# Performance work log

Hardware: AMD Instinct MI355X
Metric: run time of the kernel (lower is better)

## Reference

```python
import jax, jax.numpy as jnp
import numpy as np

B, T, D, H = 64, 256, 512, 512
COMB = D + H + D  # x, h, mask concatenated


def setup_inputs() -> dict:
    key = jax.random.key(0)
    ks = jax.random.split(key, 16)
    s = 1.0 / np.sqrt(COMB)
    sd = 1.0 / np.sqrt(D)
    inp = {
        "x": jax.random.normal(ks[0], (B, 4, T, D), dtype=jnp.float32),
        "X_mean": jax.random.normal(ks[1], (T, D), dtype=jnp.float32),
        # gate linears: stored as [in, out] so we do comb @ W + b
        "Wi": jax.random.uniform(ks[2], (COMB, H), minval=-s, maxval=s),
        "bi": jax.random.uniform(ks[3], (H,), minval=-s, maxval=s),
        "Wf": jax.random.uniform(ks[4], (COMB, H), minval=-s, maxval=s),
        "bf": jax.random.uniform(ks[5], (H,), minval=-s, maxval=s),
        "Wo": jax.random.uniform(ks[6], (COMB, H), minval=-s, maxval=s),
        "bo": jax.random.uniform(ks[7], (H,), minval=-s, maxval=s),
        "Wc": jax.random.uniform(ks[8], (COMB, H), minval=-s, maxval=s),
        "bc": jax.random.uniform(ks[9], (H,), minval=-s, maxval=s),
        # gamma_x_l: FilterLinear with identity filter -> diagonal weight + bias
        "gx_w": jax.random.uniform(ks[10], (D,), minval=-sd, maxval=sd),
        "gx_b": jax.random.uniform(ks[11], (D,), minval=-sd, maxval=sd),
        # gamma_h_l: full linear D -> D, stored [in, out]
        "gh_W": jax.random.uniform(ks[12], (D, D), minval=-sd, maxval=sd),
        "gh_b": jax.random.uniform(ks[13], (D,), minval=-sd, maxval=sd),
    }
    return inp


def _forward(x, X_mean, Wi, bi, Wf, bf, Wo, bo, Wc, bc, gx_w, gx_b, gh_W, gh_b):
    # split the packed input: each [T, B, D] for scan
    X = jnp.transpose(x[:, 0], (1, 0, 2))
    Xl = jnp.transpose(x[:, 1], (1, 0, 2))
    M = jnp.transpose(x[:, 2], (1, 0, 2))
    Dl = jnp.transpose(x[:, 3], (1, 0, 2))

    h0 = jnp.zeros((x.shape[0], H), dtype=x.dtype)
    c0 = jnp.zeros((x.shape[0], H), dtype=x.dtype)

    def step(carry, inp):
        h, c = carry
        xt, xl, m, dl, xm = inp  # xm: [D]
        delta_x = jnp.exp(-jnp.maximum(0.0, dl * gx_w + gx_b))
        delta_h = jnp.exp(-jnp.maximum(0.0, dl @ gh_W + gh_b))
        xt = m * xt + (1.0 - m) * (delta_x * xl + (1.0 - delta_x) * xm)
        h = delta_h * h
        comb = jnp.concatenate([xt, h, m], axis=-1)  # [B, COMB]
        i = jax.nn.sigmoid(comb @ Wi + bi)
        f = jax.nn.sigmoid(comb @ Wf + bf)
        o = jax.nn.sigmoid(comb @ Wo + bo)
        c_tilde = jnp.tanh(comb @ Wc + bc)
        c = f * c + i * c_tilde
        h = o * jnp.tanh(c)
        return (h, c), h

    _, outs = jax.lax.scan(step, (h0, c0), (X, Xl, M, Dl, X_mean))
    return jnp.transpose(outs, (1, 0, 2))  # [B, T, H]


def reference(x, X_mean, Wi, bi, Wf, bf, Wo, bo, Wc, bc, gx_w, gx_b, gh_W, gh_b):
    return _forward(x, X_mean, Wi, bi, Wf, bf, Wo, bo, Wc, bc, gx_w, gx_b, gh_W, gh_b)
```

## Files before the change

kernel.cpp:

```cpp
#include <hip/hip_runtime.h>
#include <hip/hip_fp16.h>
#include <math.h>

#define TT 256
#define BB 64
#define DD 512
#define HH 512
#define NC 2048

#define AH_OFF   0ull
#define DLH_OFF  8388608ull
#define DH_OFF   12582912ull
#define GP_OFF   20971520ull
#define WCT_OFF  37748736ull
#define GHT_OFF  38797312ull
#define WHT_OFF  38928384ull
#define BC_OFF   39452672ull
#define HS_OFF   39454720ull
#define FLG_OFF  39487488ull

typedef _Float16 h8_t __attribute__((ext_vector_type(8)));
typedef _Float16 h4_t __attribute__((ext_vector_type(4)));
typedef float f32x4 __attribute__((ext_vector_type(4)));
typedef unsigned long long ull2_t __attribute__((ext_vector_type(2)));

typedef const __attribute__((address_space(1))) void* gas_p;
typedef __attribute__((address_space(3))) void* las_p;

__device__ __forceinline__ float fast_exp2(float x) {
#if defined(__has_builtin)
#if __has_builtin(__builtin_amdgcn_exp2f)
  return __builtin_amdgcn_exp2f(x);
#else
  return exp2f(x);
#endif
#else
  return exp2f(x);
#endif
}
__device__ __forceinline__ float fast_rcp(float x) {
#if defined(__has_builtin)
#if __has_builtin(__builtin_amdgcn_rcpf)
  return __builtin_amdgcn_rcpf(x);
#else
  return 1.0f / x;
#endif
#else
  return 1.0f / x;
#endif
}
#define LOG2E 1.4426950408889634f
__device__ __forceinline__ float sigmoidf_(float v) {
  return fast_rcp(1.0f + fast_exp2(-LOG2E * v));
}
__device__ __forceinline__ float tanhf_(float v) {
  return 1.0f - 2.0f * fast_rcp(1.0f + fast_exp2(2.0f * LOG2E * v));
}

__global__ __launch_bounds__(256) void prep_kernel(
    const float* __restrict__ x, const float* __restrict__ Xmean,
    const float* __restrict__ gxw, const float* __restrict__ gxb,
    __half* __restrict__ AH, __half* __restrict__ DLh,
    const float* __restrict__ Wi, const float* __restrict__ bi,
    const float* __restrict__ Wf, const float* __restrict__ bff,
    const float* __restrict__ Wo, const float* __restrict__ bo,
    const float* __restrict__ Wc, const float* __restrict__ bc,
    const float* __restrict__ ghW,
    __half* __restrict__ WCT, __half* __restrict__ WHT,
    __half* __restrict__ GHT, float* __restrict__ BC,
    unsigned* __restrict__ HS) {
  const int bx = blockIdx.x;
  const int tid = threadIdx.x;

  if (bx < 8192) {
    int idx = bx * 256 + tid;
    int d = (idx & 127) * 4;
    int r = idx >> 7;
    int b = r & 63, t = r >> 6;
    size_t base = (((size_t)b * 4) * TT + t) * DD + d;
    const float4 X = *(const float4*)&x[base];
    const float4 Xl = *(const float4*)&x[base + (size_t)TT * DD];
    const float4 M = *(const float4*)&x[base + 2ull * TT * DD];
    const float4 Dl = *(const float4*)&x[base + 3ull * TT * DD];
    const float4 xm = *(const float4*)&Xmean[(size_t)t * DD + d];
    const float4 gw = *(const float4*)&gxw[d];
    const float4 gb = *(const float4*)&gxb[d];
    float o[4];
    {
      float dx = fast_exp2(-LOG2E * fmaxf(0.f, Dl.x * gw.x + gb.x));
      o[0] = M.x * X.x + (1.f - M.x) * (dx * Xl.x + (1.f - dx) * xm.x);
    }
    {
      float dx = fast_exp2(-LOG2E * fmaxf(0.f, Dl.y * gw.y + gb.y));
      o[1] = M.y * X.y + (1.f - M.y) * (dx * Xl.y + (1.f - dx) * xm.y);
    }
    {
      float dx = fast_exp2(-LOG2E * fmaxf(0.f, Dl.z * gw.z + gb.z));
      o[2] = M.z * X.z + (1.f - M.z) * (dx * Xl.z + (1.f - dx) * xm.z);
    }
    {
      float dx = fast_exp2(-LOG2E * fmaxf(0.f, Dl.w * gw.w + gb.w));
      o[3] = M.w * X.w + (1.f - M.w) * (dx * Xl.w + (1.f - dx) * xm.w);
    }
    h4_t xo = {(_Float16)o[0], (_Float16)o[1], (_Float16)o[2], (_Float16)o[3]};
    h4_t mo = {(_Float16)M.x, (_Float16)M.y, (_Float16)M.z, (_Float16)M.w};
    h4_t dlo = {(_Float16)Dl.x, (_Float16)Dl.y, (_Float16)Dl.z, (_Float16)Dl.w};
    *(h4_t*)&AH[(size_t)r * 1024 + d] = xo;
    *(h4_t*)&AH[(size_t)r * 1024 + 512 + d] = mo;
    *(h4_t*)&DLh[(size_t)r * 512 + d] = dlo;
    return;
  }

  if (bx == 9025) {
    for (int i = tid; i < 32832; i += 256) HS[i] = 0u;
    return;
  }

  const int rbx = bx - 8192;
  if (rbx == 832) {
    const float* bs[4] = {bi, bff, bo, bc};
    for (int j = tid; j < 512; j += 256)
#pragma unroll
      for (int g = 0; g < 4; ++g) BC[j * 4 + g] = bs[g][j];
    return;
  }
  __shared__ _Float16 tl[64][68];
  const int p = rbx % 13;
  const int tile = rbx / 13;
  const int k0 = (tile >> 3) << 6, j0 = (tile & 7) << 6;
  const float* Ws[4] = {Wi, Wf, Wo, Wc};

  const float* src;
  size_t koff;
  __half* dst;
  int dstride, dkoff, g = 0;
  if (p < 12) {
    g = p & 3;
    const int part = p >> 2;
    src = Ws[g];
    koff = (part == 0) ? 0 : (part == 1 ? 1024 : 512);
    if (part == 2) { dst = WHT; dstride = 512; dkoff = 0; }
    else           { dst = WCT; dstride = 1024; dkoff = (part == 1) ? 512 : 0; }
  } else {
    src = ghW; koff = 0; dst = GHT; dstride = 512; dkoff = 0;
  }

  const int jj = tid & 63, kr = tid >> 6;
#pragma unroll
  for (int r = 0; r < 16; ++r) {
    const int kk = r * 4 + kr;
    tl[jj][kk] = (_Float16)src[(koff + k0 + kk) * 512 + (j0 + jj)];
  }
  __syncthreads();

  const int c4 = (tid & 15) * 4;
#pragma unroll
  for (int pass = 0; pass < 4; ++pass) {
    const int jj2 = (tid >> 4) + pass * 16;
    const h4_t v = *(const h4_t*)&tl[jj2][c4];
    size_t idx;
    if (p < 12)
      idx = (size_t)(4 * (j0 + jj2) + g) * dstride + dkoff + k0 + c4;
    else
      idx = (size_t)(j0 + jj2) * 512 + k0 + c4;
    *(h4_t*)&dst[idx] = v;
  }
}

__device__ __forceinline__ void gemm_body(
    _Float16* Ash, _Float16* Bsh,
    const __half* __restrict__ A, const __half* __restrict__ BT,
    const float* __restrict__ bias, void* __restrict__ C,
    int K, int Ncols, int mode, int id, int nblk) {
  const int tid = threadIdx.x;
  const int lane = tid & 63, w = tid >> 6;
  const int l15 = lane & 15, quad = lane >> 4;
  const int wr = w >> 1, wc = w & 1;

  const int nx = Ncols >> 7;
  const int ny = nblk / nx;
  const int ysl = ny >> 3;
  const int xcd = id & 7;
  const int q = id >> 3;
  const int row0 = (xcd * ysl + (q % ysl)) * 128;
  const int col0 = (q / ysl) * 128;

  f32x4 acc[4][4] = {};

  const int ci0 = tid, ci1 = 256 + tid;
  const int ar0 = ci0 >> 2, ac0 = (ci0 & 3) * 8;
  const int ar1 = ci1 >> 2, ac1 = (ci1 & 3) * 8;
  const __half* Abase = A + (size_t)row0 * K;
  const __half* Bbase = BT + (size_t)col0 * K;

  for (int k0 = 0; k0 < K; k0 += 32) {
    __syncthreads();
    __builtin_amdgcn_global_load_lds((gas_p)(Abase + (size_t)ar0 * K + k0 + ac0),
                                     (las_p)(Ash + ci0 * 8), 16, 0, 0);
    __builtin_amdgcn_global_load_lds((gas_p)(Abase + (size_t)ar1 * K + k0 + ac1),
                                     (las_p)(Ash + ci1 * 8), 16, 0, 0);
    __builtin_amdgcn_global_load_lds((gas_p)(Bbase + (size_t)ar0 * K + k0 + ac0),
                                     (las_p)(Bsh + ci0 * 8), 16, 0, 0);
    __builtin_amdgcn_global_load_lds((gas_p)(Bbase + (size_t)ar1 * K + k0 + ac1),
                                     (las_p)(Bsh + ci1 * 8), 16, 0, 0);
    __syncthreads();
    h8_t af[4], bf[4];
#pragma unroll
    for (int mt = 0; mt < 4; ++mt)
      af[mt] = *(const h8_t*)&Ash[(wr * 64 + mt * 16 + l15) * 32 + quad * 8];
#pragma unroll
    for (int ct = 0; ct < 4; ++ct)
      bf[ct] = *(const h8_t*)&Bsh[(wc * 64 + ct * 16 + l15) * 32 + quad * 8];
#pragma unroll
    for (int mt = 0; mt < 4; ++mt)
#pragma unroll
      for (int ct = 0; ct < 4; ++ct)
        acc[mt][ct] = __builtin_amdgcn_mfma_f32_16x16x32_f16(af[mt], bf[ct], acc[mt][ct], 0, 0, 0);
  }

#pragma unroll
  for (int ct = 0; ct < 4; ++ct) {
    const int col = col0 + wc * 64 + ct * 16 + l15;
    const float bv = bias[col];
#pragma unroll
    for (int mt = 0; mt < 4; ++mt) {
#pragma unroll
      for (int reg = 0; reg < 4; ++reg) {
        const int row = row0 + wr * 64 + mt * 16 + quad * 4 + reg;
        float v = acc[mt][ct][reg] + bv;
        if (mode == 0) {
          ((__half*)C)[(size_t)row * Ncols + col] = __float2half(v);
        } else {
          ((float*)C)[(size_t)row * Ncols + col] = fast_exp2(-LOG2E * fmaxf(0.f, v));
        }
      }
    }
  }
}

__global__ __launch_bounds__(256, 2) void gemms_kernel(
    const __half* __restrict__ AH, const __half* __restrict__ WCT,
    const float* __restrict__ BC, __half* __restrict__ GPh,
    const __half* __restrict__ DLh, const __half* __restrict__ GHT,
    const float* __restrict__ ghb, float* __restrict__ DHp) {
  __shared__ _Float16 Ash[128 * 32];
  __shared__ _Float16 Bsh[128 * 32];
  const int id = blockIdx.x;
  if (id < 2048) {
    gemm_body(Ash, Bsh, AH, WCT, BC, (void*)GPh, 1024, NC, 0, id, 2048);
  } else {
    gemm_body(Ash, Bsh, DLh, GHT, ghb, (void*)DHp, 512, 512, 1, id - 2048, 512);
  }
}

__global__ __launch_bounds__(512)
__attribute__((amdgpu_waves_per_eu(2, 2))) void persist_rnn(
    const __half* __restrict__ GPh, const float* __restrict__ DH,
    const __half* __restrict__ WHT, unsigned* __restrict__ hs,
    int* __restrict__ flg, float* __restrict__ out) {
  __shared__ __align__(16) float gbuf[16 * 260];
  __shared__ __align__(16) unsigned long long stag[2048];
  const int g = blockIdx.x & 3;
  const int m = blockIdx.x >> 2;
  const int tid = threadIdx.x;
  const int lane = tid & 63;
  const int w = tid >> 6;
  const int l15 = lane & 15;
  const int quad = lane >> 4;
  const int rowg0 = g << 4;

  h8_t bfrag[2][16];
  const int colbase = (m << 8) + (w << 5);
#pragma unroll
  for (int nt = 0; nt < 2; ++nt) {
#pragma unroll
    for (int kt = 0; kt < 16; ++kt) {
      int col = colbase + nt * 16 + l15;
      int k = kt * 32 + quad * 8;
      bfrag[nt][kt] = *(const h8_t*)&WHT[(size_t)col * 512 + k];
    }
  }

  const int r_ep = w;
  const int ug = (m << 6) + lane;
  const int ktu = ug >> 5, q3 = (ug >> 3) & 3, qi = (ug & 7) >> 1;
  const int d0 = ktu * 256 + (q3 * 16 + r_ep) * 4 + qi;
  const int d1 = ktu * 256 + (q3 * 16 + r_ep + 8) * 4 + qi;

  float c0 = 0.f, c1 = 0.f;

  for (int t = 0; t < TT; ++t) {
#pragma unroll
    for (int nt = 0; nt < 2; ++nt)
#pragma unroll
      for (int kt = 0; kt < 16; ++kt)
        asm volatile("" : "+v"(bfrag[nt][kt]));

    const h4_t gha = *(const h4_t*)&GPh[((size_t)t * 64 + rowg0 + r_ep) * NC + (ug << 2)];
    const h4_t ghb = *(const h4_t*)&GPh[((size_t)t * 64 + rowg0 + r_ep + 8) * NC + (ug << 2)];
    const int tn = (t + 1 < TT) ? t + 1 : t;
    const float dha = DH[((size_t)tn * 64 + rowg0 + r_ep) * HH + ug];
    const float dhb = DH[((size_t)tn * 64 + rowg0 + r_ep + 8) * HH + ug];

    if (t > 0) {
      if (w == 0) {
        const int* fb = flg + (g << 4);
        for (;;) {
          int v = __hip_atomic_load(&fb[lane & 7], __ATOMIC_RELAXED,
                                    __HIP_MEMORY_SCOPE_AGENT);
          if (__all(v >= t)) break;
          __builtin_amdgcn_s_sleep(1);
        }
      }
      __syncthreads();
    }

    const unsigned long long* hsp =
        (const unsigned long long*)hs + ((size_t)(t & 1) * 4 + g) * 2048;
    unsigned long long sv0 = __hip_atomic_load(&hsp[tid], __ATOMIC_RELAXED,
                                               __HIP_MEMORY_SCOPE_AGENT);
    unsigned long long sv1 = __hip_atomic_load(&hsp[tid + 512], __ATOMIC_RELAXED,
                                               __HIP_MEMORY_SCOPE_AGENT);
    unsigned long long sv2 = __hip_atomic_load(&hsp[tid + 1024], __ATOMIC_RELAXED,
                                               __HIP_MEMORY_SCOPE_AGENT);
    unsigned long long sv3 = __hip_atomic_load(&hsp[tid + 1536], __ATOMIC_RELAXED,
                                               __HIP_MEMORY_SCOPE_AGENT);
    stag[tid] = sv0;
    stag[tid + 512] = sv1;
    stag[tid + 1024] = sv2;
    stag[tid + 1536] = sv3;
    __syncthreads();

    h8_t af[16];
#pragma unroll
    for (int kt = 0; kt < 16; ++kt) {
      ull2_t u2 = *(const ull2_t*)&stag[kt * 128 + lane * 2];
      af[kt] = __builtin_bit_cast(h8_t, u2);
    }

    f32x4 acc0 = {0.f, 0.f, 0.f, 0.f};
    f32x4 acc1 = {0.f, 0.f, 0.f, 0.f};
#pragma unroll
    for (int kt = 0; kt < 16; ++kt) {
      acc0 = __builtin_amdgcn_mfma_f32_16x16x32_f16(af[kt], bfrag[0][kt], acc0, 0, 0, 0);
      acc1 = __builtin_amdgcn_mfma_f32_16x16x32_f16(af[kt], bfrag[1][kt], acc1, 0, 0, 0);
    }
#pragma unroll
    for (int reg = 0; reg < 4; ++reg) {
      int row = quad * 4 + reg;
      gbuf[row * 260 + (w << 5) + l15] = acc0[reg];
      gbuf[row * 260 + (w << 5) + 16 + l15] = acc1[reg];
    }
    __syncthreads();

    float h0v, h1v;
    {
      const float4 gv = *(const float4*)&gbuf[r_ep * 260 + (lane << 2)];
      float ig = sigmoidf_(gv.x + (float)gha[0]);
      float fg = sigmoidf_(gv.y + (float)gha[1]);
      float og = sigmoidf_(gv.z + (float)gha[2]);
      float ct = tanhf_(gv.w + (float)gha[3]);
      c0 = fg * c0 + ig * ct;
      h0v = og * tanhf_(c0);
    }
    {
      const float4 gv = *(const float4*)&gbuf[(r_ep + 8) * 260 + (lane << 2)];
      float ig = sigmoidf_(gv.x + (float)ghb[0]);
      float fg = sigmoidf_(gv.y + (float)ghb[1]);
      float og = sigmoidf_(gv.z + (float)ghb[2]);
      float ct = tanhf_(gv.w + (float)ghb[3]);
      c1 = fg * c1 + ig * ct;
      h1v = og * tanhf_(c1);
    }

    if (t + 1 < TT) {
      unsigned* hsn = hs + ((size_t)((t + 1) & 1) * 4 + g) * 4096;
      unsigned short hb0 = __half_as_ushort(__float2half(dha * h0v));
      unsigned o0 = (unsigned)__shfl_xor((int)(unsigned)hb0, 1) & 0xffffu;
      unsigned short hb1 = __half_as_ushort(__float2half(dhb * h1v));
      unsigned o1 = (unsigned)__shfl_xor((int)(unsigned)hb1, 1) & 0xffffu;
      if (!(lane & 1)) {
        __hip_atomic_store(&hsn[d0], (unsigned)hb0 | (o0 << 16), __ATOMIC_RELAXED,
                           __HIP_MEMORY_SCOPE_AGENT);
        __hip_atomic_store(&hsn[d1], (unsigned)hb1 | (o1 << 16), __ATOMIC_RELAXED,
                           __HIP_MEMORY_SCOPE_AGENT);
      }
    }
    out[((size_t)(rowg0 + r_ep) * TT + t) * HH + ug] = h0v;
    out[((size_t)(rowg0 + r_ep + 8) * TT + t) * HH + ug] = h1v;

    __syncthreads();
    if (t + 1 < TT && tid == 0)
      __hip_atomic_store(&flg[(g << 4) + m], t + 1, __ATOMIC_RELAXED,
                         __HIP_MEMORY_SCOPE_AGENT);
  }
}

extern "C" void kernel_launch(void* const* d_in, const int* in_sizes, int n_in,
                              void* d_out, int out_size, void* d_ws,
                              size_t ws_size, hipStream_t stream) {
  const float* x = (const float*)d_in[0];
  const float* Xmean = (const float*)d_in[1];
  const float* Wi = (const float*)d_in[2];
  const float* bi = (const float*)d_in[3];
  const float* Wf = (const float*)d_in[4];
  const float* bf = (const float*)d_in[5];
  const float* Wo = (const float*)d_in[6];
  const float* bo = (const float*)d_in[7];
  const float* Wc = (const float*)d_in[8];
  const float* bc = (const float*)d_in[9];
  const float* gxw = (const float*)d_in[10];
  const float* gxb = (const float*)d_in[11];
  const float* ghW = (const float*)d_in[12];
  const float* ghb = (const float*)d_in[13];
  float* out = (float*)d_out;
  float* ws = (float*)d_ws;

  __half* AH = (__half*)(ws + AH_OFF);
  __half* DLh = (__half*)(ws + DLH_OFF);
  float* DH = ws + DH_OFF;
  __half* GPh = (__half*)(ws + GP_OFF);
  __half* WCT = (__half*)(ws + WCT_OFF);
  __half* GHT = (__half*)(ws + GHT_OFF);
  __half* WHT = (__half*)(ws + WHT_OFF);
  float* BC = ws + BC_OFF;
  unsigned* HS = (unsigned*)(ws + HS_OFF);
  int* FLG = (int*)(ws + FLG_OFF);

  prep_kernel<<<9026, 256, 0, stream>>>(x, Xmean, gxw, gxb, AH, DLh,
                                        Wi, bi, Wf, bf, Wo, bo, Wc, bc, ghW,
                                        WCT, WHT, GHT, BC, HS);
  gemms_kernel<<<2560, 256, 0, stream>>>(AH, WCT, BC, GPh, DLh, GHT, ghb, DH);
  void* args[] = {(void*)&GPh, (void*)&DH, (void*)&WHT,
                  (void*)&HS, (void*)&FLG, (void*)&out};
  hipLaunchCooperativeKernel((const void*)persist_rnn, dim3(32), dim3(512),
                             args, 0, stream);
}
```

Before: 986.7 us.

## Fuse input-projection GEMMs into persistent RNN kernel with per-timestep readiness counters

Merges the separate GEMM kernel into the cooperative persistent RNN launch. 224 extra blocks compute the input-gate and decay GEMM tiles ordered by time panel, and each finished tile bumps a counter. The 32 recurrent blocks spin on those counters before reading each step's projections, so the GEMM work overlaps the sequential recurrence instead of running before it. GEMM tiles shrink to 128x128 on 8 waves, and all stores and loads become agent-scope atomics. The trade-offs are extra polling and atomic memory traffic, and the GEMM blocks sharing CUs with the latency-critical recurrent blocks.

```diff
diff --git a/kernel.cpp b/kernel.cpp
--- a/kernel.cpp
+++ b/kernel.cpp
@@ -112,7 +112,7 @@
   }
 
   if (bx == 9025) {
-    for (int i = tid; i < 32832; i += 256) HS[i] = 0u;
+    for (int i = tid; i < 33088; i += 256) HS[i] = 0u;
     return;
   }
 
@@ -167,60 +167,46 @@
   }
 }
 
-__device__ __forceinline__ void gemm_body(
+__device__ __forceinline__ void gemm_tile(
     _Float16* Ash, _Float16* Bsh,
     const __half* __restrict__ A, const __half* __restrict__ BT,
     const float* __restrict__ bias, void* __restrict__ C,
-    int K, int Ncols, int mode, int id, int nblk) {
+    int K, int Ncols, int mode, int row0, int col0, int* cntp) {
   const int tid = threadIdx.x;
   const int lane = tid & 63, w = tid >> 6;
   const int l15 = lane & 15, quad = lane >> 4;
-  const int wr = w >> 1, wc = w & 1;
-
-  const int nx = Ncols >> 7;
-  const int ny = nblk / nx;
-  const int ysl = ny >> 3;
-  const int xcd = id & 7;
-  const int q = id >> 3;
-  const int row0 = (xcd * ysl + (q % ysl)) * 128;
-  const int col0 = (q / ysl) * 128;
-
-  f32x4 acc[4][4] = {};
-
-  const int ci0 = tid, ci1 = 256 + tid;
-  const int ar0 = ci0 >> 2, ac0 = (ci0 & 3) * 8;
-  const int ar1 = ci1 >> 2, ac1 = (ci1 & 3) * 8;
+  const int wr = w >> 2, wc = w & 3;
+
+  f32x4 acc[4][2] = {};
+
+  const int ar = tid >> 2, ac = (tid & 3) * 8;
   const __half* Abase = A + (size_t)row0 * K;
   const __half* Bbase = BT + (size_t)col0 * K;
 
   for (int k0 = 0; k0 < K; k0 += 32) {
     __syncthreads();
-    __builtin_amdgcn_global_load_lds((gas_p)(Abase + (size_t)ar0 * K + k0 + ac0),
-                                     (las_p)(Ash + ci0 * 8), 16, 0, 0);
-    __builtin_amdgcn_global_load_lds((gas_p)(Abase + (size_t)ar1 * K + k0 + ac1),
-                                     (las_p)(Ash + ci1 * 8), 16, 0, 0);
-    __builtin_amdgcn_global_load_lds((gas_p)(Bbase + (size_t)ar0 * K + k0 + ac0),
-                                     (las_p)(Bsh + ci0 * 8), 16, 0, 0);
-    __builtin_amdgcn_global_load_lds((gas_p)(Bbase + (size_t)ar1 * K + k0 + ac1),
-                                     (las_p)(Bsh + ci1 * 8), 16, 0, 0);
-    __syncthreads();
-    h8_t af[4], bf[4];
+    __builtin_amdgcn_global_load_lds((gas_p)(Abase + (size_t)ar * K + k0 + ac),
+                                     (las_p)(Ash + tid * 8), 16, 0, 0);
+    __builtin_amdgcn_global_load_lds((gas_p)(Bbase + (size_t)ar * K + k0 + ac),
+                                     (las_p)(Bsh + tid * 8), 16, 0, 0);
+    __syncthreads();
+    h8_t af[4], bf[2];
 #pragma unroll
     for (int mt = 0; mt < 4; ++mt)
       af[mt] = *(const h8_t*)&Ash[(wr * 64 + mt * 16 + l15) * 32 + quad * 8];
 #pragma unroll
-    for (int ct = 0; ct < 4; ++ct)
-      bf[ct] = *(const h8_t*)&Bsh[(wc * 64 + ct * 16 + l15) * 32 + quad * 8];
+    for (int ct = 0; ct < 2; ++ct)
+      bf[ct] = *(const h8_t*)&Bsh[(wc * 32 + ct * 16 + l15) * 32 + quad * 8];
 #pragma unroll
     for (int mt = 0; mt < 4; ++mt)
 #pragma unroll
-      for (int ct = 0; ct < 4; ++ct)
+      for (int ct = 0; ct < 2; ++ct)
         acc[mt][ct] = __builtin_amdgcn_mfma_f32_16x16x32_f16(af[mt], bf[ct], acc[mt][ct], 0, 0, 0);
   }
 
 #pragma unroll
-  for (int ct = 0; ct < 4; ++ct) {
-    const int col = col0 + wc * 64 + ct * 16 + l15;
+  for (int ct = 0; ct < 2; ++ct) {
+    const int col = col0 + wc * 32 + ct * 16 + l15;
     const float bv = bias[col];
 #pragma unroll
     for (int mt = 0; mt < 4; ++mt) {
@@ -229,37 +215,50 @@
         const int row = row0 + wr * 64 + mt * 16 + quad * 4 + reg;
         float v = acc[mt][ct][reg] + bv;
         if (mode == 0) {
-          ((__half*)C)[(size_t)row * Ncols + col] = __float2half(v);
+          __hip_atomic_store((unsigned short*)C + (size_t)row * Ncols + col,
+                             (unsigned short)__half_as_ushort(__float2half(v)),
+                             __ATOMIC_RELAXED, __HIP_MEMORY_SCOPE_AGENT);
         } else {
-          ((float*)C)[(size_t)row * Ncols + col] = fast_exp2(-LOG2E * fmaxf(0.f, v));
+          __hip_atomic_store((float*)C + (size_t)row * Ncols + col,
+                             fast_exp2(-LOG2E * fmaxf(0.f, v)),
+                             __ATOMIC_RELAXED, __HIP_MEMORY_SCOPE_AGENT);
         }
       }
     }
   }
-}
-
-__global__ __launch_bounds__(256, 2) void gemms_kernel(
+  asm volatile("s_waitcnt vmcnt(0)" ::: "memory");
+  if (lane == 0)
+    __hip_atomic_fetch_add(cntp, 1, __ATOMIC_RELAXED, __HIP_MEMORY_SCOPE_AGENT);
+}
+
+__global__ __launch_bounds__(512)
+__attribute__((amdgpu_waves_per_eu(2, 2))) void fused_kernel(
+    __half* __restrict__ GPh, float* __restrict__ DHf,
+    const __half* __restrict__ WHT, unsigned* __restrict__ hs,
+    int* __restrict__ flg, float* __restrict__ out,
     const __half* __restrict__ AH, const __half* __restrict__ WCT,
-    const float* __restrict__ BC, __half* __restrict__ GPh,
-    const __half* __restrict__ DLh, const __half* __restrict__ GHT,
-    const float* __restrict__ ghb, float* __restrict__ DHp) {
+    const float* __restrict__ BC, const __half* __restrict__ DLh,
+    const __half* __restrict__ GHT, const float* __restrict__ ghb) {
+  __shared__ __align__(16) float gbuf[16 * 260];
+  __shared__ __align__(16) unsigned long long stag[2048];
   __shared__ _Float16 Ash[128 * 32];
   __shared__ _Float16 Bsh[128 * 32];
-  const int id = blockIdx.x;
-  if (id < 2048) {
-    gemm_body(Ash, Bsh, AH, WCT, BC, (void*)GPh, 1024, NC, 0, id, 2048);
-  } else {
-    gemm_body(Ash, Bsh, DLh, GHT, ghb, (void*)DHp, 512, 512, 1, id - 2048, 512);
-  }
-}
-
-__global__ __launch_bounds__(512)
-__attribute__((amdgpu_waves_per_eu(2, 2))) void persist_rnn(
-    const __half* __restrict__ GPh, const float* __restrict__ DH,
-    const __half* __restrict__ WHT, unsigned* __restrict__ hs,
-    int* __restrict__ flg, float* __restrict__ out) {
-  __shared__ __align__(16) float gbuf[16 * 260];
-  __shared__ __align__(16) unsigned long long stag[2048];
+  int* cnt = flg + 64;
+
+  if (blockIdx.x >= 32) {
+    const int pp = blockIdx.x - 32;
+    for (int tau = pp; tau < 2560; tau += 224) {
+      const int p = tau / 20, i = tau % 20;
+      if (i < 4)
+        gemm_tile(Ash, Bsh, DLh, GHT, ghb, (void*)DHf, 512, 512, 1,
+                  p * 128, i * 128, &cnt[128 + p]);
+      else
+        gemm_tile(Ash, Bsh, AH, WCT, BC, (void*)GPh, 1024, NC, 0,
+                  p * 128, (i - 4) * 128, &cnt[p]);
+    }
+    return;
+  }
+
   const int g = blockIdx.x & 3;
   const int m = blockIdx.x >> 2;
   const int tid = threadIdx.x;
@@ -287,6 +286,8 @@
   const int d0 = ktu * 256 + (q3 * 16 + r_ep) * 4 + qi;
   const int d1 = ktu * 256 + (q3 * 16 + r_ep + 8) * 4 + qi;
 
+  const unsigned long long* gp64 = (const unsigned long long*)GPh;
+
   float c0 = 0.f, c1 = 0.f;
 
   for (int t = 0; t < TT; ++t) {
@@ -296,24 +297,39 @@
       for (int kt = 0; kt < 16; ++kt)
         asm volatile("" : "+v"(bfrag[nt][kt]));
 
-    const h4_t gha = *(const h4_t*)&GPh[((size_t)t * 64 + rowg0 + r_ep) * NC + (ug << 2)];
-    const h4_t ghb = *(const h4_t*)&GPh[((size_t)t * 64 + rowg0 + r_ep + 8) * NC + (ug << 2)];
     const int tn = (t + 1 < TT) ? t + 1 : t;
-    const float dha = DH[((size_t)tn * 64 + rowg0 + r_ep) * HH + ug];
-    const float dhb = DH[((size_t)tn * 64 + rowg0 + r_ep + 8) * HH + ug];
-
-    if (t > 0) {
-      if (w == 0) {
-        const int* fb = flg + (g << 4);
-        for (;;) {
-          int v = __hip_atomic_load(&fb[lane & 7], __ATOMIC_RELAXED,
-                                    __HIP_MEMORY_SCOPE_AGENT);
-          if (__all(v >= t)) break;
-          __builtin_amdgcn_s_sleep(1);
-        }
+    const int pG = t >> 1, pD = tn >> 1;
+
+    if (w == 0) {
+      const int* fb = flg + (g << 4);
+      for (;;) {
+        int ok = (__hip_atomic_load(&cnt[pG], __ATOMIC_RELAXED,
+                                    __HIP_MEMORY_SCOPE_AGENT) >= 128) &
+                 (__hip_atomic_load(&cnt[128 + pD], __ATOMIC_RELAXED,
+                                    __HIP_MEMORY_SCOPE_AGENT) >= 32);
+        if (t > 0)
+          ok &= (__hip_atomic_load(&fb[lane & 7], __ATOMIC_RELAXED,
+                                   __HIP_MEMORY_SCOPE_AGENT) >= t);
+        if (__all(ok)) break;
+        __builtin_amdgcn_s_sleep(1);
       }
-      __syncthreads();
-    }
+    }
+    __syncthreads();
+
+    const h4_t gha = __builtin_bit_cast(
+        h4_t, __hip_atomic_load(
+                  &gp64[((size_t)t * 64 + rowg0 + r_ep) * (NC / 4) + ug],
+                  __ATOMIC_RELAXED, __HIP_MEMORY_SCOPE_AGENT));
+    const h4_t ghb_ = __builtin_bit_cast(
+        h4_t, __hip_atomic_load(
+                  &gp64[((size_t)t * 64 + rowg0 + r_ep + 8) * (NC / 4) + ug],
+                  __ATOMIC_RELAXED, __HIP_MEMORY_SCOPE_AGENT));
+    const float dha =
+        __hip_atomic_load(&DHf[((size_t)tn * 64 + rowg0 + r_ep) * HH + ug],
+                          __ATOMIC_RELAXED, __HIP_MEMORY_SCOPE_AGENT);
+    const float dhb =
+        __hip_atomic_load(&DHf[((size_t)tn * 64 + rowg0 + r_ep + 8) * HH + ug],
+                          __ATOMIC_RELAXED, __HIP_MEMORY_SCOPE_AGENT);
 
     const unsigned long long* hsp =
         (const unsigned long long*)hs + ((size_t)(t & 1) * 4 + g) * 2048;
@@ -365,10 +381,10 @@
     }
     {
       const float4 gv = *(const float4*)&gbuf[(r_ep + 8) * 260 + (lane << 2)];
-      float ig = sigmoidf_(gv.x + (float)ghb[0]);
-      float fg = sigmoidf_(gv.y + (float)ghb[1]);
-      float og = sigmoidf_(gv.z + (float)ghb[2]);
-      float ct = tanhf_(gv.w + (float)ghb[3]);
+      float ig = sigmoidf_(gv.x + (float)ghb_[0]);
+      float fg = sigmoidf_(gv.y + (float)ghb_[1]);
+      float og = sigmoidf_(gv.z + (float)ghb_[2]);
+      float ct = tanhf_(gv.w + (float)ghb_[3]);
       c1 = fg * c1 + ig * ct;
       h1v = og * tanhf_(c1);
     }
@@ -430,9 +446,9 @@
   prep_kernel<<<9026, 256, 0, stream>>>(x, Xmean, gxw, gxb, AH, DLh,
                                         Wi, bi, Wf, bf, Wo, bo, Wc, bc, ghW,
                                         WCT, WHT, GHT, BC, HS);
-  gemms_kernel<<<2560, 256, 0, stream>>>(AH, WCT, BC, GPh, DLh, GHT, ghb, DH);
-  void* args[] = {(void*)&GPh, (void*)&DH, (void*)&WHT,
-                  (void*)&HS, (void*)&FLG, (void*)&out};
-  hipLaunchCooperativeKernel((const void*)persist_rnn, dim3(32), dim3(512),
+  void* args[] = {(void*)&GPh, (void*)&DH,  (void*)&WHT, (void*)&HS,
+                  (void*)&FLG, (void*)&out, (void*)&AH,  (void*)&WCT,
+                  (void*)&BC,  (void*)&DLh, (void*)&GHT, (void*)&ghb};
+  hipLaunchCooperativeKernel((const void*)fused_kernel, dim3(256), dim3(512),
                              args, 0, stream);
 }
```

Measured after the change: 1.030 ms. 4.4% more time.

## Use 256x256 GEMM tiles with double-buffered LDS staging in input-projection GEMMs

Applied to the files above, without the earlier changes.

The precompute GEMMs move from 128x128 tiles on 256-thread blocks to 256x256 tiles on 512-thread blocks. A two-slot LDS buffer lets the next K-slice load through global_load_lds while MFMAs run on the current one, so each iteration needs one barrier instead of two. Larger tiles cut global traffic per flop. The cost is fewer blocks (640 instead of 2560), which may underfill the GPU, plus more accumulator registers per wave. The GEMMs are only part of the total time, since the persistent RNN kernel remains.

```diff
diff --git a/kernel.cpp b/kernel.cpp
--- a/kernel.cpp
+++ b/kernel.cpp
@@ -167,67 +167,98 @@
   }
 }
 
-__device__ __forceinline__ void gemm_body(
-    _Float16* Ash, _Float16* Bsh,
-    const __half* __restrict__ A, const __half* __restrict__ BT,
-    const float* __restrict__ bias, void* __restrict__ C,
-    int K, int Ncols, int mode, int id, int nblk) {
+__global__ __launch_bounds__(512)
+__attribute__((amdgpu_waves_per_eu(2, 2))) void gemms_kernel(
+    const __half* __restrict__ AH, const __half* __restrict__ WCT,
+    const float* __restrict__ BC, __half* __restrict__ GPh,
+    const __half* __restrict__ DLh, const __half* __restrict__ GHT,
+    const float* __restrict__ ghb, float* __restrict__ DHp) {
+  __shared__ _Float16 Ash[2][8192];
+  __shared__ _Float16 Bsh[2][8192];
+  const int bid = blockIdx.x;
+  const __half* A;
+  const __half* BT;
+  const float* bias;
+  void* C;
+  int K, Ncols, mode, id, nblk;
+  if (bid < 512) {
+    A = AH; BT = WCT; bias = BC; C = (void*)GPh;
+    K = 1024; Ncols = 2048; mode = 0; id = bid; nblk = 512;
+  } else {
+    A = DLh; BT = GHT; bias = ghb; C = (void*)DHp;
+    K = 512; Ncols = 512; mode = 1; id = bid - 512; nblk = 128;
+  }
+
   const int tid = threadIdx.x;
   const int lane = tid & 63, w = tid >> 6;
   const int l15 = lane & 15, quad = lane >> 4;
-  const int wr = w >> 1, wc = w & 1;
-
-  const int nx = Ncols >> 7;
+  const int wr = w >> 2, wc = w & 3;
+
+  const int nx = Ncols >> 8;
   const int ny = nblk / nx;
   const int ysl = ny >> 3;
   const int xcd = id & 7;
   const int q = id >> 3;
-  const int row0 = (xcd * ysl + (q % ysl)) * 128;
-  const int col0 = (q / ysl) * 128;
-
-  f32x4 acc[4][4] = {};
-
-  const int ci0 = tid, ci1 = 256 + tid;
-  const int ar0 = ci0 >> 2, ac0 = (ci0 & 3) * 8;
-  const int ar1 = ci1 >> 2, ac1 = (ci1 & 3) * 8;
+  const int row0 = (xcd * ysl + (q % ysl)) * 256;
+  const int col0 = (q / ysl) * 256;
+
+  f32x4 acc[8][4] = {};
+
+  const int ar0 = tid >> 2, ac0 = (tid & 3) * 8;
+  const int ar1 = 128 + (tid >> 2), ac1 = (tid & 3) * 8;
   const __half* Abase = A + (size_t)row0 * K;
   const __half* Bbase = BT + (size_t)col0 * K;
 
-  for (int k0 = 0; k0 < K; k0 += 32) {
+#define STAGE_TILE(slot, k0)                                                   \
+  do {                                                                         \
+    __builtin_amdgcn_global_load_lds(                                          \
+        (gas_p)(Abase + (size_t)ar0 * K + (k0) + ac0),                         \
+        (las_p)(&Ash[slot][(size_t)tid * 8]), 16, 0, 0);                       \
+    __builtin_amdgcn_global_load_lds(                                          \
+        (gas_p)(Abase + (size_t)ar1 * K + (k0) + ac1),                         \
+        (las_p)(&Ash[slot][(size_t)(512 + tid) * 8]), 16, 0, 0);               \
+    __builtin_amdgcn_global_load_lds(                                          \
+        (gas_p)(Bbase + (size_t)ar0 * K + (k0) + ac0),                         \
+        (las_p)(&Bsh[slot][(size_t)tid * 8]), 16, 0, 0);                       \
+    __builtin_amdgcn_global_load_lds(                                          \
+        (gas_p)(Bbase + (size_t)ar1 * K + (k0) + ac1),                         \
+        (las_p)(&Bsh[slot][(size_t)(512 + tid) * 8]), 16, 0, 0);               \
+  } while (0)
+
+  const int nt = K >> 5;
+  int cur = 0;
+  STAGE_TILE(0, 0);
+  __syncthreads();
+
+  for (int t = 0; t < nt; ++t) {
+    if (t + 1 < nt) STAGE_TILE(cur ^ 1, (t + 1) << 5);
+    h8_t af[8], bf[4];
+#pragma unroll
+    for (int mf = 0; mf < 8; ++mf)
+      af[mf] = *(const h8_t*)&Ash[cur][(wr * 128 + mf * 16 + l15) * 32 + quad * 8];
+#pragma unroll
+    for (int nf = 0; nf < 4; ++nf)
+      bf[nf] = *(const h8_t*)&Bsh[cur][(wc * 64 + nf * 16 + l15) * 32 + quad * 8];
+#pragma unroll
+    for (int mf = 0; mf < 8; ++mf)
+#pragma unroll
+      for (int nf = 0; nf < 4; ++nf)
+        acc[mf][nf] = __builtin_amdgcn_mfma_f32_16x16x32_f16(af[mf], bf[nf], acc[mf][nf], 0, 0, 0);
     __syncthreads();
-    __builtin_amdgcn_global_load_lds((gas_p)(Abase + (size_t)ar0 * K + k0 + ac0),
-                                     (las_p)(Ash + ci0 * 8), 16, 0, 0);
-    __builtin_amdgcn_global_load_lds((gas_p)(Abase + (size_t)ar1 * K + k0 + ac1),
-                                     (las_p)(Ash + ci1 * 8), 16, 0, 0);
-    __builtin_amdgcn_global_load_lds((gas_p)(Bbase + (size_t)ar0 * K + k0 + ac0),
-                                     (las_p)(Bsh + ci0 * 8), 16, 0, 0);
-    __builtin_amdgcn_global_load_lds((gas_p)(Bbase + (size_t)ar1 * K + k0 + ac1),
-                                     (las_p)(Bsh + ci1 * 8), 16, 0, 0);
-    __syncthreads();
-    h8_t af[4], bf[4];
-#pragma unroll
-    for (int mt = 0; mt < 4; ++mt)
-      af[mt] = *(const h8_t*)&Ash[(wr * 64 + mt * 16 + l15) * 32 + quad * 8];
-#pragma unroll
-    for (int ct = 0; ct < 4; ++ct)
-      bf[ct] = *(const h8_t*)&Bsh[(wc * 64 + ct * 16 + l15) * 32 + quad * 8];
-#pragma unroll
-    for (int mt = 0; mt < 4; ++mt)
-#pragma unroll
-      for (int ct = 0; ct < 4; ++ct)
-        acc[mt][ct] = __builtin_amdgcn_mfma_f32_16x16x32_f16(af[mt], bf[ct], acc[mt][ct], 0, 0, 0);
-  }
-
-#pragma unroll
-  for (int ct = 0; ct < 4; ++ct) {
-    const int col = col0 + wc * 64 + ct * 16 + l15;
+    cur ^= 1;
+  }
+#undef STAGE_TILE
+
+#pragma unroll
+  for (int nf = 0; nf < 4; ++nf) {
+    const int col = col0 + wc * 64 + nf * 16 + l15;
     const float bv = bias[col];
 #pragma unroll
-    for (int mt = 0; mt < 4; ++mt) {
+    for (int mf = 0; mf < 8; ++mf) {
 #pragma unroll
       for (int reg = 0; reg < 4; ++reg) {
-        const int row = row0 + wr * 64 + mt * 16 + quad * 4 + reg;
-        float v = acc[mt][ct][reg] + bv;
+        const int row = row0 + wr * 128 + mf * 16 + quad * 4 + reg;
+        float v = acc[mf][nf][reg] + bv;
         if (mode == 0) {
           ((__half*)C)[(size_t)row * Ncols + col] = __float2half(v);
         } else {
@@ -235,21 +266,6 @@
         }
       }
     }
-  }
-}
-
-__global__ __launch_bounds__(256, 2) void gemms_kernel(
-    const __half* __restrict__ AH, const __half* __restrict__ WCT,
-    const float* __restrict__ BC, __half* __restrict__ GPh,
-    const __half* __restrict__ DLh, const __half* __restrict__ GHT,
-    const float* __restrict__ ghb, float* __restrict__ DHp) {
-  __shared__ _Float16 Ash[128 * 32];
-  __shared__ _Float16 Bsh[128 * 32];
-  const int id = blockIdx.x;
-  if (id < 2048) {
-    gemm_body(Ash, Bsh, AH, WCT, BC, (void*)GPh, 1024, NC, 0, id, 2048);
-  } else {
-    gemm_body(Ash, Bsh, DLh, GHT, ghb, (void*)DHp, 512, 512, 1, id - 2048, 512);
   }
 }
 
@@ -430,7 +446,7 @@
   prep_kernel<<<9026, 256, 0, stream>>>(x, Xmean, gxw, gxb, AH, DLh,
                                         Wi, bi, Wf, bf, Wo, bo, Wc, bc, ghW,
                                         WCT, WHT, GHT, BC, HS);
-  gemms_kernel<<<2560, 256, 0, stream>>>(AH, WCT, BC, GPh, DLh, GHT, ghb, DH);
+  gemms_kernel<<<640, 512, 0, stream>>>(AH, WCT, BC, GPh, DLh, GHT, ghb, DH);
   void* args[] = {(void*)&GPh, (void*)&DH, (void*)&WHT,
                   (void*)&HS, (void*)&FLG, (void*)&out};
   hipLaunchCooperativeKernel((const void*)persist_rnn, dim3(32), dim3(512),
```

Measured after the change: 1.061 ms. +7.5%, slower.
